# Kernel optimization log

Hardware: AMD Instinct MI355X
Metric: run time of the kernel (lower is better)

Reference implementation:

```python
import jax, jax.numpy as jnp
import numpy as np

B, T, D = 1, 2048, 2048
HQ, HKV = 32, 8
DH = D // HQ          # 64
NREP = HQ // HKV      # 4


def _apply_rope(x, cos, sin):
    # x: (B, T, H, DH); cos/sin: (T, DH//2). Complex multiply on interleaved pairs:
    # (x0 + i*x1) * (c + i*s) -> (x0*c - x1*s, x0*s + x1*c)
    b, t, h, d = x.shape
    xr = x.reshape(b, t, h, d // 2, 2)
    x0, x1 = xr[..., 0], xr[..., 1]
    c = cos[:t][None, :, None, :]
    s = sin[:t][None, :, None, :]
    o0 = x0 * c - x1 * s
    o1 = x0 * s + x1 * c
    return jnp.stack([o0, o1], axis=-1).reshape(b, t, h, d)


def setup_inputs() -> dict:
    key = jax.random.key(0)
    ks = jax.random.split(key, 6)
    w = 0.02
    x = jax.random.normal(ks[0], (B, T, D), dtype=jnp.float32)
    Wq = jax.random.normal(ks[1], (HQ * DH, D), dtype=jnp.float32) * w
    Wk = jax.random.normal(ks[2], (HKV * DH, D), dtype=jnp.float32) * w
    Wv = jax.random.normal(ks[3], (HKV * DH, D), dtype=jnp.float32) * w
    Wo = jax.random.normal(ks[4], (D, HQ * DH), dtype=jnp.float32) * w
    # standard RoPE frequencies, theta = 10000
    inv_freq = 1.0 / (10000.0 ** (np.arange(0, DH, 2, dtype=np.float32) / DH))
    angles = np.arange(T, dtype=np.float32)[:, None] * inv_freq[None, :]  # (T, DH//2)
    rope_cos = jnp.asarray(np.cos(angles))
    rope_sin = jnp.asarray(np.sin(angles))
    mask = jnp.tril(jnp.ones((T, T), dtype=bool))  # causal
    return {"x": x, "Wq": Wq, "Wk": Wk, "Wv": Wv, "Wo": Wo,
            "rope_cos": rope_cos, "rope_sin": rope_sin, "mask": mask}


def reference(x, Wq, Wk, Wv, Wo, rope_cos, rope_sin, mask):
    b, t, d = x.shape
    q = (x @ Wq.T).reshape(b, t, HQ, DH)
    k = (x @ Wk.T).reshape(b, t, HKV, DH)
    v = (x @ Wv.T).reshape(b, t, HKV, DH)
    q = _apply_rope(q, rope_cos, rope_sin)
    k = _apply_rope(k, rope_cos, rope_sin)
    # GQA: head index = kv_head * NREP + rep (matches torch expand+reshape order)
    qg = q.reshape(b, t, HKV, NREP, DH)
    scale = jnp.sqrt(jnp.float32(DH))
    # scores: (B, HKV, NREP, T, S) without materializing expanded K
    scores = jnp.einsum('bthrd,bshd->bhrts', qg, k) / scale
    scores = jnp.where(mask[None, None, None, :t, :t], scores, -jnp.inf)
    attn = jax.nn.softmax(scores, axis=-1)
    out = jnp.einsum('bhrts,bshd->bthrd', attn, v)  # (B, T, HKV, NREP, DH)
    out = out.reshape(b, t, HQ * DH)
    return out @ Wo.T
```

## Files before the change

### kernel.cpp

```cpp
#include <hip/hip_runtime.h>
#include <math.h>
#include <stdint.h>

static constexpr int T   = 2048;
static constexpr int D   = 2048;
static constexpr int HQ  = 32;
static constexpr int HKV = 8;
static constexpr int DH  = 64;
static constexpr int DKV = HKV * DH;
static constexpr int NQKV = D + 2 * DKV;

typedef float f32x4 __attribute__((ext_vector_type(4)));
typedef __bf16 bf16x8 __attribute__((ext_vector_type(8)));
typedef __bf16 bf16x2 __attribute__((ext_vector_type(2)));
typedef unsigned short u16x8 __attribute__((ext_vector_type(8)));
typedef unsigned short u16x4 __attribute__((ext_vector_type(4)));

__device__ __forceinline__ unsigned short f2bf(float f) {
  union { float f; unsigned u; } v; v.f = f;
  unsigned u = v.u;
  return (unsigned short)((u + 0x7FFFu + ((u >> 16) & 1u)) >> 16);
}
__device__ __forceinline__ float bf2f(unsigned short b) {
  union { unsigned u; float f; } v; v.u = ((unsigned)b) << 16;
  return v.f;
}
__device__ __forceinline__ unsigned pk2bf(float a, float b) {
#if __has_builtin(__builtin_amdgcn_cvt_pk_bf16_f32)
  bf16x2 r = __builtin_amdgcn_cvt_pk_bf16_f32(a, b);
  return __builtin_bit_cast(unsigned, r);
#else
  return (unsigned)f2bf(a) | ((unsigned)f2bf(b) << 16);
#endif
}
__device__ __forceinline__ float fexp2(float x) {
#if __has_builtin(__builtin_amdgcn_exp2f)
  return __builtin_amdgcn_exp2f(x);
#else
  return exp2f(x);
#endif
}
__device__ __forceinline__ float frcp(float x) {
#if __has_builtin(__builtin_amdgcn_rcpf)
  return __builtin_amdgcn_rcpf(x);
#else
  return 1.0f / x;
#endif
}
__device__ __forceinline__ f32x4 mfma16(u16x8 a, u16x8 b, f32x4 c) {
  return __builtin_amdgcn_mfma_f32_16x16x32_bf16(
      __builtin_bit_cast(bf16x8, a), __builtin_bit_cast(bf16x8, b), c, 0, 0, 0);
}
__device__ __forceinline__ void gld16(const unsigned short* g, unsigned short* l) {
  __builtin_amdgcn_global_load_lds(
      (const __attribute__((address_space(1))) unsigned*)g,
      (__attribute__((address_space(3))) unsigned*)l, 16, 0, 0);
}

__global__ __launch_bounds__(256) void cvt_all(const float* __restrict__ x,
                                               const float* __restrict__ Wq,
                                               const float* __restrict__ Wk,
                                               const float* __restrict__ Wv,
                                               const float* __restrict__ Wo,
                                               unsigned short* __restrict__ xb,
                                               unsigned short* __restrict__ wqkv,
                                               unsigned short* __restrict__ wob) {
  int b = blockIdx.x;
  const float* src;
  unsigned short* dst;
  if (b < 2048)      { src = x;  dst = xb; }
  else if (b < 4096) { src = Wq; dst = wqkv;                          b -= 2048; }
  else if (b < 4608) { src = Wk; dst = wqkv + (size_t)D * D;          b -= 4096; }
  else if (b < 5120) { src = Wv; dst = wqkv + (size_t)(D + DKV) * D;  b -= 4608; }
  else               { src = Wo; dst = wob;                           b -= 5120; }
  size_t i = ((size_t)b * 256 + threadIdx.x) * 8;
  float4 a = *(const float4*)(src + i);
  float4 c = *(const float4*)(src + i + 4);
  uint4 r = {pk2bf(a.x, a.y), pk2bf(a.z, a.w), pk2bf(c.x, c.y), pk2bf(c.z, c.w)};
  *(uint4*)(dst + i) = r;
}

template <bool OUT_BF16>
__global__ __launch_bounds__(256) void gemm_bt_bf16(const unsigned short* __restrict__ A,
                                                    const unsigned short* __restrict__ Bt,
                                                    void* __restrict__ Cv,
                                                    int N, int K) {
  __shared__ alignas(16) unsigned short As[64 * 128];
  __shared__ alignas(16) unsigned short Bs[128 * 128];

  const int bn = blockIdx.x * 128, bm = blockIdx.y * 64;
  const int tid = threadIdx.x, w = tid >> 6, lane = tid & 63;
  const int c = lane & 15, quad = lane >> 4;

  const int r4 = lane >> 4, ch = lane & 15;
  const unsigned short* aRow = A + (size_t)(bm + w * 16 + r4) * K;
  const unsigned short* bRow = Bt + (size_t)(bn + w * 32 + r4) * K;
  unsigned short* AsW = As + (w * 16) * 128;
  unsigned short* BsW = Bs + (w * 32) * 128;

  f32x4 acc[4][2] = {};

  for (int k0 = 0; k0 < K; k0 += 128) {
#pragma unroll
    for (int j = 0; j < 4; j++) {
      const int sch = ch ^ ((j * 4 + r4) & 15);
      gld16(aRow + (size_t)(j * 4) * K + k0 + sch * 8, AsW + j * 4 * 128);
    }
#pragma unroll
    for (int j = 0; j < 8; j++) {
      const int sch = ch ^ ((j * 4 + r4) & 15);
      gld16(bRow + (size_t)(j * 4) * K + k0 + sch * 8, BsW + j * 4 * 128);
    }
    __syncthreads();

#pragma unroll
    for (int ks = 0; ks < 4; ks++) {
      const int slot = (ks * 4 + quad) ^ c;
      u16x8 a[4], b[2];
#pragma unroll
      for (int mi = 0; mi < 4; mi++)
        a[mi] = *(const u16x8*)&As[(mi * 16 + c) * 128 + slot * 8];
#pragma unroll
      for (int ni = 0; ni < 2; ni++)
        b[ni] = *(const u16x8*)&Bs[(w * 32 + ni * 16 + c) * 128 + slot * 8];
#pragma unroll
      for (int mi = 0; mi < 4; mi++)
#pragma unroll
        for (int ni = 0; ni < 2; ni++)
          acc[mi][ni] = mfma16(a[mi], b[ni], acc[mi][ni]);
    }
    __syncthreads();
  }

#pragma unroll
  for (int mi = 0; mi < 4; mi++)
#pragma unroll
    for (int ni = 0; ni < 2; ni++)
#pragma unroll
      for (int r = 0; r < 4; r++) {
        size_t row = (size_t)(bm + mi * 16 + quad * 4 + r);
        size_t col = (size_t)(bn + w * 32 + ni * 16 + c);
        if (OUT_BF16)
          ((unsigned short*)Cv)[row * N + col] = f2bf(acc[mi][ni][r]);
        else
          ((float*)Cv)[row * N + col] = acc[mi][ni][r];
      }
}

__global__ __launch_bounds__(256) void rope_tv(unsigned short* __restrict__ QKV,
                                               const float* __restrict__ cosb,
                                               const float* __restrict__ sinb,
                                               unsigned short* __restrict__ VT) {
  const int QP = T * HQ * (DH / 2);
  if (blockIdx.x < 10240) {
    int idx = blockIdx.x * 256 + threadIdx.x;
    unsigned short* p;
    int t, i;
    float sc;
    if (idx < QP) {
      t = idx / (HQ * DH / 2);
      int rem = idx - t * (HQ * DH / 2);
      i = rem & 31;
      p = QKV + (size_t)t * NQKV + rem * 2;
      sc = 0.125f * 1.44269504088896340736f;
    } else {
      int j = idx - QP;
      t = j / (HKV * DH / 2);
      int rem = j - t * (HKV * DH / 2);
      i = rem & 31;
      p = QKV + (size_t)t * NQKV + D + rem * 2;
      sc = 1.0f;
    }
    float x0 = bf2f(p[0]), x1 = bf2f(p[1]);
    float cs = cosb[t * 32 + i], sn = sinb[t * 32 + i];
    *(unsigned*)p = pk2bf((x0 * cs - x1 * sn) * sc, (x0 * sn + x1 * cs) * sc);
  } else {
    __shared__ unsigned short Ts[64][65];
    const int bid = blockIdx.x - 10240;
    const int tb = bid & 31, db = bid >> 5;
    const int tid = threadIdx.x;
    const int r = tid >> 2, c0 = (tid & 3) * 16;
    const unsigned short* src = QKV + (size_t)(tb * 64 + r) * NQKV + (D + DKV) + db * 64 + c0;
    *(u16x8*)&Ts[r][c0]     = *(const u16x8*)src;
    *(u16x8*)&Ts[r][c0 + 8] = *(const u16x8*)(src + 8);
    __syncthreads();
    u16x8 a, b;
#pragma unroll
    for (int j = 0; j < 8; j++) a[j] = Ts[c0 + j][r];
#pragma unroll
    for (int j = 0; j < 8; j++) b[j] = Ts[c0 + 8 + j][r];
    unsigned short* dst = VT + (size_t)(db * 64 + r) * T + tb * 64 + c0;
    *(u16x8*)dst = a;
    *(u16x8*)(dst + 8) = b;
  }
}

__global__ __launch_bounds__(256) void attn_kernel(const unsigned short* __restrict__ QKV,
                                                   const unsigned short* __restrict__ VT,
                                                   unsigned short* __restrict__ Ob) {
  const int kh = blockIdx.x;
  const int qt = (int)(gridDim.y - 1 - blockIdx.y);
  const int qbase = qt * 16;
  const int tid = threadIdx.x, w = tid >> 6, lane = tid & 63;
  const int c = lane & 15, quad = lane >> 4;
  const int h = kh * 4 + w;

  __shared__ alignas(16) unsigned short Kt[2][64 * 64];
  __shared__ alignas(16) unsigned short Vt[2][64 * 64];
  __shared__ alignas(16) unsigned short Pb[4 * 16 * 72];

  unsigned short* PbW = Pb + w * 16 * 72;

  u16x8 qf[2];
  {
    const unsigned short* qp = QKV + (size_t)(qbase + c) * NQKV + h * DH + quad * 8;
    qf[0] = *(const u16x8*)qp;
    qf[1] = *(const u16x8*)(qp + 32);
  }

  const int srow = lane >> 3;
  const int sch  = (lane & 7) ^ srow;
  const unsigned short* kgBase = QKV + D + (size_t)(w * 16 + srow) * NQKV + kh * DH + sch * 8;
  const unsigned short* vgBase = VT + (size_t)(kh * DH + w * 16 + srow) * T + sch * 8;

  f32x4 o[4] = {};
  float l = 0.f;

  const int nFull = qt >> 2;

#pragma unroll
  for (int j = 0; j < 2; j++) {
    gld16(kgBase + (size_t)(j * 8) * NQKV, &Kt[0][(w * 16 + j * 8) * 64]);
    gld16(vgBase + (size_t)(j * 8) * T, &Vt[0][(w * 16 + j * 8) * 64]);
  }

  for (int st = 0; st <= nFull; st++) {
    const int cur = st & 1;
    __syncthreads();
    if (st < nFull) {
#pragma unroll
      for (int j = 0; j < 2; j++) {
        gld16(kgBase + ((size_t)(st + 1) * 64 + (size_t)j * 8) * NQKV,
              &Kt[cur ^ 1][(w * 16 + j * 8) * 64]);
        gld16(vgBase + (size_t)(j * 8) * T + (st + 1) * 64,
              &Vt[cur ^ 1][(w * 16 + j * 8) * 64]);
      }
    }

    f32x4 sacc[4] = {};
#pragma unroll
    for (int ks = 0; ks < 2; ks++) {
#pragma unroll
      for (int ni = 0; ni < 4; ni++) {
        const int slot = (ks * 4 + quad) ^ (c & 7);
        u16x8 kf = *(const u16x8*)&Kt[cur][(ni * 16 + c) * 64 + slot * 8];
        sacc[ni] = mfma16(kf, qf[ks], sacc[ni]);
      }
    }

    if (st == nFull) {
      const int qrow = qbase + c;
#pragma unroll
      for (int ni = 0; ni < 4; ni++)
#pragma unroll
        for (int r = 0; r < 4; r++) {
          int key = st * 64 + ni * 16 + quad * 4 + r;
          if (key > qrow) sacc[ni][r] = -INFINITY;
        }
    }

#pragma unroll
    for (int ni = 0; ni < 4; ni++) {
      float p0 = fexp2(sacc[ni][0]);
      float p1 = fexp2(sacc[ni][1]);
      float p2 = fexp2(sacc[ni][2]);
      float p3 = fexp2(sacc[ni][3]);
      l += (p0 + p1) + (p2 + p3);
      uint2 pr = {pk2bf(p0, p1), pk2bf(p2, p3)};
      *(uint2*)&PbW[c * 72 + ni * 16 + quad * 4] = pr;
    }

#pragma unroll
    for (int ks = 0; ks < 2; ks++) {
      u16x8 pf = *(const u16x8*)&PbW[c * 72 + ks * 32 + quad * 8];
#pragma unroll
      for (int ni = 0; ni < 4; ni++) {
        const int slot = (ks * 4 + quad) ^ (c & 7);
        u16x8 vf = *(const u16x8*)&Vt[cur][(ni * 16 + c) * 64 + slot * 8];
        o[ni] = mfma16(pf, vf, o[ni]);
      }
    }
  }

  l += __shfl_xor(l, 16, 64);
  l += __shfl_xor(l, 32, 64);

  float lR[4];
#pragma unroll
  for (int r = 0; r < 4; r++) lR[r] = frcp(__shfl(l, quad * 4 + r, 64));
#pragma unroll
  for (int ni = 0; ni < 4; ni++)
#pragma unroll
    for (int r = 0; r < 4; r++) {
      size_t row = (size_t)(qbase + quad * 4 + r);
      size_t col = (size_t)(h * DH + ni * 16 + c);
      Ob[row * D + col] = f2bf(o[ni][r] * lR[r]);
    }
}

extern "C" void kernel_launch(void* const* d_in, const int* in_sizes, int n_in,
                              void* d_out, int out_size, void* d_ws, size_t ws_size,
                              hipStream_t stream) {
  const float* x  = (const float*)d_in[0];
  const float* Wq = (const float*)d_in[1];
  const float* Wk = (const float*)d_in[2];
  const float* Wv = (const float*)d_in[3];
  const float* Wo = (const float*)d_in[4];
  const float* rc = (const float*)d_in[5];
  const float* rs = (const float*)d_in[6];
  float* out = (float*)d_out;

  char* ws = (char*)d_ws;
  unsigned short* xb   = (unsigned short*)(ws);
  unsigned short* wqkv = (unsigned short*)(ws + (size_t)(8u  << 20));
  unsigned short* wob  = (unsigned short*)(ws + (size_t)(20u << 20));
  unsigned short* qkvb = (unsigned short*)(ws + (size_t)(28u << 20));
  unsigned short* Ab   = xb;
  unsigned short* VT   = wqkv;

  cvt_all<<<dim3(7168), 256, 0, stream>>>(x, Wq, Wk, Wv, Wo, xb, wqkv, wob);

  gemm_bt_bf16<true><<<dim3(NQKV / 128, T / 64), 256, 0, stream>>>(xb, wqkv, qkvb, NQKV, D);

  rope_tv<<<dim3(10240 + 256), 256, 0, stream>>>(qkvb, rc, rs, VT);

  attn_kernel<<<dim3(HKV, T / 16), 256, 0, stream>>>(qkvb, VT, Ab);

  gemm_bt_bf16<false><<<dim3(D / 128, T / 64), 256, 0, stream>>>(Ab, wob, out, D, D);
}
```

Before: 221.0 us.

## Load V fragments directly from global into registers, drop V LDS staging

The attention kernel stops staging V tiles in double-buffered shared memory. Each wave now reads its V MFMA fragments straight from the transposed V buffer in global memory into registers at the start of each key tile. It also raises MFMA wave priority with s_setprio around the matmul loops and sets a min-blocks-per-CU launch bound of 4. This halves LDS use and removes the LDS reads for V, in exchange for redundant global/L2 reads across the four waves and exposed load latency, since V is no longer prefetched one tile ahead.

```diff
diff --git a/kernel.cpp b/kernel.cpp
--- a/kernel.cpp
+++ b/kernel.cpp
@@ -195,9 +195,9 @@
   }
 }
 
-__global__ __launch_bounds__(256) void attn_kernel(const unsigned short* __restrict__ QKV,
-                                                   const unsigned short* __restrict__ VT,
-                                                   unsigned short* __restrict__ Ob) {
+__global__ __launch_bounds__(256, 4) void attn_kernel(const unsigned short* __restrict__ QKV,
+                                                      const unsigned short* __restrict__ VT,
+                                                      unsigned short* __restrict__ Ob) {
   const int kh = blockIdx.x;
   const int qt = (int)(gridDim.y - 1 - blockIdx.y);
   const int qbase = qt * 16;
@@ -206,7 +206,6 @@
   const int h = kh * 4 + w;
 
   __shared__ alignas(16) unsigned short Kt[2][64 * 64];
-  __shared__ alignas(16) unsigned short Vt[2][64 * 64];
   __shared__ alignas(16) unsigned short Pb[4 * 16 * 72];
 
   unsigned short* PbW = Pb + w * 16 * 72;
@@ -221,7 +220,7 @@
   const int srow = lane >> 3;
   const int sch  = (lane & 7) ^ srow;
   const unsigned short* kgBase = QKV + D + (size_t)(w * 16 + srow) * NQKV + kh * DH + sch * 8;
-  const unsigned short* vgBase = VT + (size_t)(kh * DH + w * 16 + srow) * T + sch * 8;
+  const unsigned short* vBase = VT + (size_t)(kh * DH + c) * T + quad * 8;
 
   f32x4 o[4] = {};
   float l = 0.f;
@@ -229,25 +228,29 @@
   const int nFull = qt >> 2;
 
 #pragma unroll
-  for (int j = 0; j < 2; j++) {
+  for (int j = 0; j < 2; j++)
     gld16(kgBase + (size_t)(j * 8) * NQKV, &Kt[0][(w * 16 + j * 8) * 64]);
-    gld16(vgBase + (size_t)(j * 8) * T, &Vt[0][(w * 16 + j * 8) * 64]);
-  }
 
   for (int st = 0; st <= nFull; st++) {
     const int cur = st & 1;
     __syncthreads();
+
+    u16x8 vf[2][4];
+#pragma unroll
+    for (int ks = 0; ks < 2; ks++)
+#pragma unroll
+      for (int ni = 0; ni < 4; ni++)
+        vf[ks][ni] = *(const u16x8*)(vBase + (size_t)(ni * 16) * T + st * 64 + ks * 32);
+
     if (st < nFull) {
 #pragma unroll
-      for (int j = 0; j < 2; j++) {
+      for (int j = 0; j < 2; j++)
         gld16(kgBase + ((size_t)(st + 1) * 64 + (size_t)j * 8) * NQKV,
               &Kt[cur ^ 1][(w * 16 + j * 8) * 64]);
-        gld16(vgBase + (size_t)(j * 8) * T + (st + 1) * 64,
-              &Vt[cur ^ 1][(w * 16 + j * 8) * 64]);
-      }
     }
 
     f32x4 sacc[4] = {};
+    __builtin_amdgcn_s_setprio(1);
 #pragma unroll
     for (int ks = 0; ks < 2; ks++) {
 #pragma unroll
@@ -257,6 +260,7 @@
         sacc[ni] = mfma16(kf, qf[ks], sacc[ni]);
       }
     }
+    __builtin_amdgcn_s_setprio(0);
 
     if (st == nFull) {
       const int qrow = qbase + c;
@@ -283,12 +287,11 @@
 #pragma unroll
     for (int ks = 0; ks < 2; ks++) {
       u16x8 pf = *(const u16x8*)&PbW[c * 72 + ks * 32 + quad * 8];
-#pragma unroll
-      for (int ni = 0; ni < 4; ni++) {
-        const int slot = (ks * 4 + quad) ^ (c & 7);
-        u16x8 vf = *(const u16x8*)&Vt[cur][(ni * 16 + c) * 64 + slot * 8];
-        o[ni] = mfma16(pf, vf, o[ni]);
-      }
+      __builtin_amdgcn_s_setprio(1);
+#pragma unroll
+      for (int ni = 0; ni < 4; ni++)
+        o[ni] = mfma16(pf, vf[ks][ni], o[ni]);
+      __builtin_amdgcn_s_setprio(0);
     }
   }
 
```

Result: slower. 257.7 us (+16.6%).

## Fuse RoPE into QKV GEMM epilogue and raise MFMA wave priority in attention

Applied to the files above, without the earlier changes.

Applies RoPE and the Q scaling directly in the QKV GEMM epilogue. The rotation partner comes from a lane shuffle, so the separate RoPE pass that re-read and re-wrote Q and K in bf16 is gone. The V transpose now runs as its own small kernel. Attention MFMA sections are wrapped in s_setprio to favour matrix issue. The fused epilogue does scattered cos/sin loads per element, and rotating fp32 accumulators before rounding changes rounding slightly.

```diff
diff --git a/kernel.cpp b/kernel.cpp
--- a/kernel.cpp
+++ b/kernel.cpp
@@ -80,11 +80,13 @@
   *(uint4*)(dst + i) = r;
 }
 
-template <bool OUT_BF16>
+template <int EPI>
 __global__ __launch_bounds__(256) void gemm_bt_bf16(const unsigned short* __restrict__ A,
                                                     const unsigned short* __restrict__ Bt,
                                                     void* __restrict__ Cv,
-                                                    int N, int K) {
+                                                    int N, int K,
+                                                    const float* __restrict__ cosb,
+                                                    const float* __restrict__ sinb) {
   __shared__ alignas(16) unsigned short As[64 * 128];
   __shared__ alignas(16) unsigned short Bs[128 * 128];
 
@@ -132,67 +134,69 @@
     __syncthreads();
   }
 
-#pragma unroll
-  for (int mi = 0; mi < 4; mi++)
-#pragma unroll
-    for (int ni = 0; ni < 2; ni++)
-#pragma unroll
-      for (int r = 0; r < 4; r++) {
-        size_t row = (size_t)(bm + mi * 16 + quad * 4 + r);
-        size_t col = (size_t)(bn + w * 32 + ni * 16 + c);
-        if (OUT_BF16)
+  if (EPI == 0) {
+#pragma unroll
+    for (int mi = 0; mi < 4; mi++)
+#pragma unroll
+      for (int ni = 0; ni < 2; ni++)
+#pragma unroll
+        for (int r = 0; r < 4; r++) {
+          size_t row = (size_t)(bm + mi * 16 + quad * 4 + r);
+          size_t col = (size_t)(bn + w * 32 + ni * 16 + c);
+          ((float*)Cv)[row * N + col] = acc[mi][ni][r];
+        }
+  } else if (bn < 2560) {
+    const float sc = (bn < 2048) ? 0.125f * 1.44269504088896340736f : 1.0f;
+    const float sgn = (c & 1) ? 1.0f : -1.0f;
+#pragma unroll
+    for (int mi = 0; mi < 4; mi++)
+#pragma unroll
+      for (int ni = 0; ni < 2; ni++) {
+        const int i = ((w * 32 + ni * 16 + c) & 63) >> 1;
+#pragma unroll
+        for (int r = 0; r < 4; r++) {
+          const int t = bm + mi * 16 + quad * 4 + r;
+          const float cs = cosb[t * 32 + i];
+          const float sn = sinb[t * 32 + i];
+          const float val = acc[mi][ni][r];
+          const float px = __shfl_xor(val, 1, 64);
+          const float outv = (val * cs + sgn * px * sn) * sc;
+          ((unsigned short*)Cv)[(size_t)t * N + bn + w * 32 + ni * 16 + c] = f2bf(outv);
+        }
+      }
+  } else {
+#pragma unroll
+    for (int mi = 0; mi < 4; mi++)
+#pragma unroll
+      for (int ni = 0; ni < 2; ni++)
+#pragma unroll
+        for (int r = 0; r < 4; r++) {
+          size_t row = (size_t)(bm + mi * 16 + quad * 4 + r);
+          size_t col = (size_t)(bn + w * 32 + ni * 16 + c);
           ((unsigned short*)Cv)[row * N + col] = f2bf(acc[mi][ni][r]);
-        else
-          ((float*)Cv)[row * N + col] = acc[mi][ni][r];
-      }
-}
-
-__global__ __launch_bounds__(256) void rope_tv(unsigned short* __restrict__ QKV,
-                                               const float* __restrict__ cosb,
-                                               const float* __restrict__ sinb,
+        }
+  }
+}
+
+__global__ __launch_bounds__(256) void vt_only(const unsigned short* __restrict__ QKV,
                                                unsigned short* __restrict__ VT) {
-  const int QP = T * HQ * (DH / 2);
-  if (blockIdx.x < 10240) {
-    int idx = blockIdx.x * 256 + threadIdx.x;
-    unsigned short* p;
-    int t, i;
-    float sc;
-    if (idx < QP) {
-      t = idx / (HQ * DH / 2);
-      int rem = idx - t * (HQ * DH / 2);
-      i = rem & 31;
-      p = QKV + (size_t)t * NQKV + rem * 2;
-      sc = 0.125f * 1.44269504088896340736f;
-    } else {
-      int j = idx - QP;
-      t = j / (HKV * DH / 2);
-      int rem = j - t * (HKV * DH / 2);
-      i = rem & 31;
-      p = QKV + (size_t)t * NQKV + D + rem * 2;
-      sc = 1.0f;
-    }
-    float x0 = bf2f(p[0]), x1 = bf2f(p[1]);
-    float cs = cosb[t * 32 + i], sn = sinb[t * 32 + i];
-    *(unsigned*)p = pk2bf((x0 * cs - x1 * sn) * sc, (x0 * sn + x1 * cs) * sc);
-  } else {
-    __shared__ unsigned short Ts[64][65];
-    const int bid = blockIdx.x - 10240;
-    const int tb = bid & 31, db = bid >> 5;
-    const int tid = threadIdx.x;
-    const int r = tid >> 2, c0 = (tid & 3) * 16;
-    const unsigned short* src = QKV + (size_t)(tb * 64 + r) * NQKV + (D + DKV) + db * 64 + c0;
-    *(u16x8*)&Ts[r][c0]     = *(const u16x8*)src;
-    *(u16x8*)&Ts[r][c0 + 8] = *(const u16x8*)(src + 8);
-    __syncthreads();
-    u16x8 a, b;
-#pragma unroll
-    for (int j = 0; j < 8; j++) a[j] = Ts[c0 + j][r];
-#pragma unroll
-    for (int j = 0; j < 8; j++) b[j] = Ts[c0 + 8 + j][r];
-    unsigned short* dst = VT + (size_t)(db * 64 + r) * T + tb * 64 + c0;
-    *(u16x8*)dst = a;
-    *(u16x8*)(dst + 8) = b;
-  }
+  __shared__ unsigned short Ts[64][65];
+  const int bid = blockIdx.x;
+  const int tb = bid & 31, db = bid >> 5;
+  const int tid = threadIdx.x;
+  const int r = tid >> 2, c0 = (tid & 3) * 16;
+  const unsigned short* src = QKV + (size_t)(tb * 64 + r) * NQKV + (D + DKV) + db * 64 + c0;
+  *(u16x8*)&Ts[r][c0]     = *(const u16x8*)src;
+  *(u16x8*)&Ts[r][c0 + 8] = *(const u16x8*)(src + 8);
+  __syncthreads();
+  u16x8 a, b;
+#pragma unroll
+  for (int j = 0; j < 8; j++) a[j] = Ts[c0 + j][r];
+#pragma unroll
+  for (int j = 0; j < 8; j++) b[j] = Ts[c0 + 8 + j][r];
+  unsigned short* dst = VT + (size_t)(db * 64 + r) * T + tb * 64 + c0;
+  *(u16x8*)dst = a;
+  *(u16x8*)(dst + 8) = b;
 }
 
 __global__ __launch_bounds__(256) void attn_kernel(const unsigned short* __restrict__ QKV,
@@ -248,6 +252,7 @@
     }
 
     f32x4 sacc[4] = {};
+    __builtin_amdgcn_s_setprio(1);
 #pragma unroll
     for (int ks = 0; ks < 2; ks++) {
 #pragma unroll
@@ -257,6 +262,7 @@
         sacc[ni] = mfma16(kf, qf[ks], sacc[ni]);
       }
     }
+    __builtin_amdgcn_s_setprio(0);
 
     if (st == nFull) {
       const int qrow = qbase + c;
@@ -283,12 +289,14 @@
 #pragma unroll
     for (int ks = 0; ks < 2; ks++) {
       u16x8 pf = *(const u16x8*)&PbW[c * 72 + ks * 32 + quad * 8];
+      __builtin_amdgcn_s_setprio(1);
 #pragma unroll
       for (int ni = 0; ni < 4; ni++) {
         const int slot = (ks * 4 + quad) ^ (c & 7);
         u16x8 vf = *(const u16x8*)&Vt[cur][(ni * 16 + c) * 64 + slot * 8];
         o[ni] = mfma16(pf, vf, o[ni]);
       }
+      __builtin_amdgcn_s_setprio(0);
     }
   }
 
@@ -330,11 +338,13 @@
 
   cvt_all<<<dim3(7168), 256, 0, stream>>>(x, Wq, Wk, Wv, Wo, xb, wqkv, wob);
 
-  gemm_bt_bf16<true><<<dim3(NQKV / 128, T / 64), 256, 0, stream>>>(xb, wqkv, qkvb, NQKV, D);
-
-  rope_tv<<<dim3(10240 + 256), 256, 0, stream>>>(qkvb, rc, rs, VT);
+  gemm_bt_bf16<1><<<dim3(NQKV / 128, T / 64), 256, 0, stream>>>(xb, wqkv, qkvb,
+                                                                NQKV, D, rc, rs);
+
+  vt_only<<<dim3(256), 256, 0, stream>>>(qkvb, VT);
 
   attn_kernel<<<dim3(HKV, T / 16), 256, 0, stream>>>(qkvb, VT, Ab);
 
-  gemm_bt_bf16<false><<<dim3(D / 128, T / 64), 256, 0, stream>>>(Ab, wob, out, D, D);
-}
+  gemm_bt_bf16<0><<<dim3(D / 128, T / 64), 256, 0, stream>>>(Ab, wob, out, D, D,
+                                                             nullptr, nullptr);
+}
```

Result: no change. 217.7 us (-1.5%).
